# Performance work log

Hardware: AMD Instinct MI355X
Metric: run time of the kernel (lower is better)

The kernel has to match this reference:

```python
import jax, jax.numpy as jnp
import numpy as np

N = 4096      # nodes
DIM = 256     # in/out channels
H = 8         # heads
C = DIM       # per-head channels (PyG TransformerConv: out_channels per head)
EPS = 1e-5    # LayerNorm eps
P_EDGE = 0.01 # adjacency density -> avg in-degree ~41


def setup_inputs() -> dict:
    key = jax.random.key(0)
    ks = jax.random.split(key, 12)
    x = jax.random.normal(ks[0], (1, N, DIM), jnp.float32)
    # sparse random graph encoded densely (dense_to_sparse extracts nonzeros)
    adj_mat = (jax.random.uniform(ks[1], (1, N, N)) < P_EDGE).astype(jnp.float32)
    s = 1.0 / np.sqrt(DIM)
    Wq = jax.random.normal(ks[2], (DIM, H * C), jnp.float32) * s
    Wk = jax.random.normal(ks[3], (DIM, H * C), jnp.float32) * s
    Wv = jax.random.normal(ks[4], (DIM, H * C), jnp.float32) * s
    bq = jax.random.normal(ks[5], (H * C,), jnp.float32) * 0.01
    bk = jax.random.normal(ks[6], (H * C,), jnp.float32) * 0.01
    bv = jax.random.normal(ks[7], (H * C,), jnp.float32) * 0.01
    Wskip = jax.random.normal(ks[8], (DIM, DIM), jnp.float32) * s
    bskip = jax.random.normal(ks[9], (DIM,), jnp.float32) * 0.01
    gamma = jnp.ones((DIM,), jnp.float32)
    beta = jnp.zeros((DIM,), jnp.float32)
    return dict(x=x, adj_mat=adj_mat, Wq=Wq, bq=bq, Wk=Wk, bk=bk, Wv=Wv, bv=bv,
                Wskip=Wskip, bskip=bskip, gamma=gamma, beta=beta)


def reference(x, adj_mat, Wq, bq, Wk, bk, Wv, bv, Wskip, bskip, gamma, beta):
    xs = x[0]            # [N, DIM]
    adj = adj_mat[0]     # [N, N]; adj[j, i] != 0 => edge j -> i (source_to_target)
    q = (xs @ Wq + bq).reshape(N, H, C)
    k = (xs @ Wk + bk).reshape(N, H, C)
    v = (xs @ Wv + bv).reshape(N, H, C)
    # scaled dot-product attention restricted to graph edges
    scores = jnp.einsum('ihc,jhc->hij', q, k) / jnp.sqrt(jnp.float32(C))  # [H,N,N]
    mask = (adj.T != 0.0)[None]  # [1, i_target, j_source]
    neg = jnp.finfo(scores.dtype).min
    attn = jax.nn.softmax(jnp.where(mask, scores, neg), axis=-1)
    # nodes with no in-edges aggregate zero messages (scatter semantics)
    has_nbr = mask.any(axis=-1, keepdims=True)  # [1, N, 1]
    attn = jnp.where(has_nbr, attn, 0.0)
    agg = jnp.einsum('hij,jhc->ihc', attn, v)  # [N, H, C]
    out = agg.mean(axis=1)                      # concat=False -> head mean, [N, DIM]
    out = out + xs @ Wskip + bskip              # root_weight skip connection
    mu = out.mean(axis=-1, keepdims=True)
    var = ((out - mu) ** 2).mean(axis=-1, keepdims=True)
    out = (out - mu) * jax.lax.rsqrt(var + EPS) * gamma + beta  # LayerNorm
    out = out + xs                               # residual
    return out[None]  # [1, N, DIM]
```

## Files before the change

kernel.cpp:

```cpp
#include <hip/hip_runtime.h>
#include <hip/hip_bf16.h>

#define NN   4096
#define DIMM 256
#define HH   8
#define HC   2048
#define CAP  128

#define QSCALE 15.875f
#define SSCALE (0.0625f / (QSCALE * QSCALE))

typedef short    bf16x8 __attribute__((ext_vector_type(8)));
typedef float    f32x4  __attribute__((ext_vector_type(4)));
typedef float    f32x2  __attribute__((ext_vector_type(2)));

__device__ __forceinline__ float bfbits(unsigned int u) {
  union { unsigned int u; float f; } un; un.u = u; return un.f;
}
__device__ __forceinline__ unsigned short f2bf(float f) {
  union { float f; unsigned int u; } un; un.f = f;
  unsigned int r = un.u + 0x7fffu + ((un.u >> 16) & 1u);
  return (unsigned short)(r >> 16);
}
__device__ __forceinline__ int sdot4(unsigned int a, unsigned int b, int c) {
#if __has_builtin(__builtin_amdgcn_sdot4)
  return __builtin_amdgcn_sdot4((int)a, (int)b, c, false);
#else
  c += (int)(signed char)(a)       * (int)(signed char)(b);
  c += (int)(signed char)(a >> 8)  * (int)(signed char)(b >> 8);
  c += (int)(signed char)(a >> 16) * (int)(signed char)(b >> 16);
  c += (int)(signed char)(a >> 24) * (int)(signed char)(b >> 24);
  return c;
#endif
}
__device__ __forceinline__ void gload16(const void* g, void* l) {
  __builtin_amdgcn_global_load_lds(
      (const __attribute__((address_space(1))) unsigned int*)g,
      (__attribute__((address_space(3))) unsigned int*)l, 16, 0, 0);
}

__global__ __launch_bounds__(256) void build_edges_kernel(
    const float4* __restrict__ adj4, int* __restrict__ deg, int* __restrict__ nbr) {
  const int stride = gridDim.x * blockDim.x;
  for (int e4 = blockIdx.x * blockDim.x + threadIdx.x; e4 < NN * NN / 4; e4 += stride) {
    const float4 a = adj4[e4];
    if (a.x != 0.f || a.y != 0.f || a.z != 0.f || a.w != 0.f) {
      const int e = e4 << 2;
      const int j = e >> 12;
      const int ib = e & (NN - 1);
      if (a.x != 0.f) { int s = atomicAdd(&deg[ib + 0], 1); if (s < CAP) nbr[(ib + 0) * CAP + s] = j; }
      if (a.y != 0.f) { int s = atomicAdd(&deg[ib + 1], 1); if (s < CAP) nbr[(ib + 1) * CAP + s] = j; }
      if (a.z != 0.f) { int s = atomicAdd(&deg[ib + 2], 1); if (s < CAP) nbr[(ib + 2) * CAP + s] = j; }
      if (a.w != 0.f) { int s = atomicAdd(&deg[ib + 3], 1); if (s < CAP) nbr[(ib + 3) * CAP + s] = j; }
    }
  }
}

__global__ __launch_bounds__(128) void sort_nbr_kernel(
    const int* __restrict__ deg, int* __restrict__ nbr) {
  const int i = blockIdx.x, t = threadIdx.x;
  __shared__ int sl[CAP];
  int d = deg[i];
  if (d > CAP) d = CAP;
  if (d <= 1) return;
  sl[t] = (t < d) ? nbr[i * CAP + t] : 0x7fffffff;
  __syncthreads();
  for (int ksz = 2; ksz <= CAP; ksz <<= 1) {
    for (int jsz = ksz >> 1; jsz > 0; jsz >>= 1) {
      const int ixj = t ^ jsz;
      if (ixj > t) {
        const int a = sl[t], b = sl[ixj];
        const bool up = ((t & ksz) == 0);
        if ((up && a > b) || (!up && a < b)) { sl[t] = b; sl[ixj] = a; }
      }
      __syncthreads();
    }
  }
  if (t < d) nbr[i * CAP + t] = sl[t];
}

__global__ __launch_bounds__(256) void cast_x_kernel(
    const float* __restrict__ x, unsigned short* __restrict__ xb) {
  const int gid = blockIdx.x * 256 + threadIdx.x;
  const int m = gid >> 5, c = gid & 31;
  const float4 a = *(const float4*)&x[(size_t)m * 256 + c * 8];
  const float4 b = *(const float4*)&x[(size_t)m * 256 + c * 8 + 4];
  union { unsigned short u[8]; uint4 v; } o;
  o.u[0] = f2bf(a.x); o.u[1] = f2bf(a.y); o.u[2] = f2bf(a.z); o.u[3] = f2bf(a.w);
  o.u[4] = f2bf(b.x); o.u[5] = f2bf(b.y); o.u[6] = f2bf(b.z); o.u[7] = f2bf(b.w);
  const int cs = (c & 24) | ((c & 7) ^ (m & 7));
  *(uint4*)&xb[(size_t)m * 256 + cs * 8] = o.v;
}

__global__ __launch_bounds__(256) void tcast_w_kernel(
    const float* __restrict__ W0, const float* __restrict__ W1,
    const float* __restrict__ W2, unsigned short* __restrict__ T0,
    unsigned short* __restrict__ T1, unsigned short* __restrict__ T2, int Nw) {
  const float* W = blockIdx.z == 0 ? W0 : blockIdx.z == 1 ? W1 : W2;
  unsigned short* T = blockIdx.z == 0 ? T0 : blockIdx.z == 1 ? T1 : T2;
  __shared__ float Tf[64][68];
  const int t = threadIdx.x;
  const int n0 = blockIdx.x * 64, k0 = blockIdx.y * 64;
  const int kk0 = t >> 4, nc = t & 15;
#pragma unroll
  for (int r = 0; r < 4; ++r) {
    const int kk = kk0 + r * 16;
    const float4 a = *(const float4*)&W[(size_t)(k0 + kk) * Nw + n0 + nc * 4];
    Tf[kk][nc * 4 + 0] = a.x; Tf[kk][nc * 4 + 1] = a.y;
    Tf[kk][nc * 4 + 2] = a.z; Tf[kk][nc * 4 + 3] = a.w;
  }
  __syncthreads();
  const int n = t >> 2, cp = t & 3;
#pragma unroll
  for (int qq = 0; qq < 2; ++qq) {
    const int cc = cp * 2 + qq;
    union { unsigned short u[8]; uint4 v; } o;
#pragma unroll
    for (int e = 0; e < 8; ++e) o.u[e] = f2bf(Tf[cc * 8 + e][n]);
    const int ng = n0 + n;
    const int co = cc ^ (ng & 7);
    *(uint4*)&T[(size_t)ng * 256 + blockIdx.y * 64 + co * 8] = o.v;
  }
}

template <int MODE>
__global__ __launch_bounds__(256) void mfma_gemm_kernel(
    const unsigned short* __restrict__ Abf,
    const unsigned short* __restrict__ B0, const unsigned short* __restrict__ B1,
    const unsigned short* __restrict__ B2,
    const float* __restrict__ bias0, const float* __restrict__ bias1,
    const float* __restrict__ bias2,
    void* __restrict__ C0v, void* __restrict__ C1v, void* __restrict__ C2v,
    int Nc) {
  const unsigned short* Bm = blockIdx.z == 0 ? B0 : blockIdx.z == 1 ? B1 : B2;
  const float* bias = blockIdx.z == 0 ? bias0 : blockIdx.z == 1 ? bias1 : bias2;
  void* Cv = blockIdx.z == 0 ? C0v : blockIdx.z == 1 ? C1v : C2v;

  __shared__ unsigned short lds[2 * 128 * 64];
  unsigned short* As = lds;
  unsigned short* Bs = lds + 128 * 64;

  const int t = threadIdx.x, l = t & 63, w = t >> 6;
  const int m0 = blockIdx.y * 128, n0 = blockIdx.x * 128;
  const int wm = w >> 1, wn = w & 1;

  const f32x4 zero = {0.f, 0.f, 0.f, 0.f};
  f32x4 acc[4][4];
#pragma unroll
  for (int fm = 0; fm < 4; ++fm)
#pragma unroll
    for (int fn = 0; fn < 4; ++fn) acc[fm][fn] = zero;

  for (int kb = 0; kb < 4; ++kb) {
#pragma unroll
    for (int r = 0; r < 4; ++r) {
      const int rr = r * 8 + (l >> 3), ch = l & 7;
      gload16(Abf + (size_t)(m0 + w * 32 + rr) * 256 + kb * 64 + ch * 8,
              As + w * 2048 + r * 512);
      gload16(Bm + (size_t)(n0 + w * 32 + rr) * 256 + kb * 64 + ch * 8,
              Bs + w * 2048 + r * 512);
    }
    __syncthreads();

#pragma unroll
    for (int s = 0; s < 2; ++s) {
      const int chab = (4 * s + (l >> 4)) ^ (l & 7);
      bf16x8 af[4], bfr[4];
#pragma unroll
      for (int fm = 0; fm < 4; ++fm) {
        const int row = wm * 64 + fm * 16 + (l & 15);
        af[fm] = *(const bf16x8*)&As[row * 64 + chab * 8];
      }
#pragma unroll
      for (int fn = 0; fn < 4; ++fn) {
        const int row = wn * 64 + fn * 16 + (l & 15);
        bfr[fn] = *(const bf16x8*)&Bs[row * 64 + chab * 8];
      }
#pragma unroll
      for (int fm = 0; fm < 4; ++fm)
#pragma unroll
        for (int fn = 0; fn < 4; ++fn)
          acc[fm][fn] = __builtin_amdgcn_mfma_f32_16x16x32_bf16(
              af[fm], bfr[fn], acc[fm][fn], 0, 0, 0);
    }
    __syncthreads();
  }

  float bv[4];
#pragma unroll
  for (int fn = 0; fn < 4; ++fn) bv[fn] = bias[n0 + wn * 64 + fn * 16 + (l & 15)];

  if (MODE == 1) {
    const bool is_i8 = blockIdx.z < 2;
    unsigned char* lds8 = (unsigned char*)lds;
    unsigned char* Cc8 = (unsigned char*)Cv;
#pragma unroll
    for (int fm = 0; fm < 4; ++fm) {
      const int col = wn * 64 + (l & 15);
#pragma unroll
      for (int fn = 0; fn < 4; ++fn) {
#pragma unroll
        for (int r = 0; r < 4; ++r) {
          const int row = wm * 64 + fm * 16 + (l >> 4) * 4 + r;
          const float val = acc[fm][fn][r] + bv[fn];
          unsigned char ob;
          if (is_i8) {
            int vi = (int)rintf(val * QSCALE);
            vi = vi < -127 ? -127 : (vi > 127 ? 127 : vi);
            ob = (unsigned char)(signed char)vi;
          } else {
            const unsigned int pk = __builtin_amdgcn_cvt_pk_fp8_f32(val, val, 0, false);
            ob = (unsigned char)(pk & 0xff);
          }
          lds8[row * 128 + col + fn * 16] = ob;
        }
      }
    }
    __syncthreads();
#pragma unroll
    for (int r2 = 0; r2 < 4; ++r2) {
      const int idx = r2 * 256 + t;
      const int row = idx >> 3, colb = (idx & 7) * 16;
      *(uint4*)&Cc8[(size_t)(m0 + row) * Nc + n0 + colb] =
          *(const uint4*)&lds8[row * 128 + colb];
    }
  } else {
    float* Cc = (float*)Cv;
#pragma unroll
    for (int fm = 0; fm < 4; ++fm)
#pragma unroll
      for (int fn = 0; fn < 4; ++fn)
#pragma unroll
        for (int r = 0; r < 4; ++r) {
          const int row = wm * 64 + fm * 16 + (l >> 4) * 4 + r;
          const int col = wn * 64 + fn * 16 + (l & 15);
          Cc[(size_t)(m0 + row) * Nc + n0 + col] = acc[fm][fn][r] + bv[fn];
        }
  }
}

__global__ __launch_bounds__(256) void attn_ln_kernel(
    const unsigned char* __restrict__ q8, const unsigned char* __restrict__ k8,
    const unsigned char* __restrict__ v8, const float* __restrict__ skip,
    const float* __restrict__ x, const int* __restrict__ deg,
    const int* __restrict__ nbr, const float* __restrict__ gamma,
    const float* __restrict__ beta, float* __restrict__ out) {
  const int i = blockIdx.x;
  const int t = threadIdx.x;
  const int lane = t & 63, wave = t >> 6;
  const int h = lane >> 3, sub = lane & 7;

  __shared__ int slist[CAP];
  __shared__ float sc[CAP * HH];
  __shared__ float wacc[4][2][DIMM];
  __shared__ float mred[HH], lred[HH];
  __shared__ float w1[4], w2[4];

  int d = deg[i];
  if (d > CAP) d = CAP;

  if (t < CAP) slist[t] = (t < d) ? nbr[i * CAP + t] : 0;

  uint4 Q0, Q1;
  {
    const uint4* qp = (const uint4*)&q8[(size_t)i * HC + (h << 8) + (sub << 5)];
    Q0 = qp[0]; Q1 = qp[1];
  }
  __syncthreads();

  {
    const size_t hoff = (size_t)(h << 8) + (sub << 5);
    int n = wave;
    uint4 a0, a1, b0, b1;
    if (n < d) {
      const uint4* kp = (const uint4*)&k8[(size_t)slist[n] * HC + hoff];
      a0 = kp[0]; a1 = kp[1];
    }
    if (n + 4 < d) {
      const uint4* kp = (const uint4*)&k8[(size_t)slist[n + 4] * HC + hoff];
      b0 = kp[0]; b1 = kp[1];
    }
    while (n < d) {
      uint4 c0, c1;
      if (n + 8 < d) {
        const uint4* kp = (const uint4*)&k8[(size_t)slist[n + 8] * HC + hoff];
        c0 = kp[0]; c1 = kp[1];
      }
      int iacc = 0;
      iacc = sdot4(a0.x, Q0.x, iacc); iacc = sdot4(a0.y, Q0.y, iacc);
      iacc = sdot4(a0.z, Q0.z, iacc); iacc = sdot4(a0.w, Q0.w, iacc);
      iacc = sdot4(a1.x, Q1.x, iacc); iacc = sdot4(a1.y, Q1.y, iacc);
      iacc = sdot4(a1.z, Q1.z, iacc); iacc = sdot4(a1.w, Q1.w, iacc);
      float s = (float)iacc;
      s += __shfl_xor(s, 1);
      s += __shfl_xor(s, 2);
      s += __shfl_xor(s, 4);
      if (sub == 0) sc[n * HH + h] = s * SSCALE;
      a0 = b0; a1 = b1; b0 = c0; b1 = c1;
      n += 4;
    }
  }
  __syncthreads();

  if (t < 64) {
    const int h2i = t >> 3, s2 = t & 7;
    float m = -1e30f;
    for (int n2 = s2; n2 < d; n2 += 8) m = fmaxf(m, sc[n2 * HH + h2i]);
    m = fmaxf(m, __shfl_xor(m, 1));
    m = fmaxf(m, __shfl_xor(m, 2));
    m = fmaxf(m, __shfl_xor(m, 4));
    float lsum = 0.f;
    for (int n2 = s2; n2 < d; n2 += 8) lsum += expf(sc[n2 * HH + h2i] - m);
    lsum += __shfl_xor(lsum, 1);
    lsum += __shfl_xor(lsum, 2);
    lsum += __shfl_xor(lsum, 4);
    if (s2 == 0) { mred[h2i] = m; lred[h2i] = (lsum > 0.f) ? 1.f / lsum : 0.f; }
  }
  __syncthreads();

  for (int e = t; e < d * HH; e += 256) {
    const int hh = e & (HH - 1);
    sc[e] = expf(sc[e] - mred[hh]) * lred[hh];
  }
  __syncthreads();

  float a[8] = {0.f, 0.f, 0.f, 0.f, 0.f, 0.f, 0.f, 0.f};
  const int g = lane >> 5, c8 = lane & 31;
  {
    const size_t voff = (size_t)(g * 4) * 256 + (size_t)c8 * 8;
    int n = wave;
    uint2 A0, A1, A2, A3, B0v, B1v, B2v, B3v;
    if (n < d) {
      const unsigned char* vr = &v8[(size_t)slist[n] * HC + voff];
      A0 = *(const uint2*)(vr + 0 * 256); A1 = *(const uint2*)(vr + 1 * 256);
      A2 = *(const uint2*)(vr + 2 * 256); A3 = *(const uint2*)(vr + 3 * 256);
    }
    if (n + 4 < d) {
      const unsigned char* vr = &v8[(size_t)slist[n + 4] * HC + voff];
      B0v = *(const uint2*)(vr + 0 * 256); B1v = *(const uint2*)(vr + 1 * 256);
      B2v = *(const uint2*)(vr + 2 * 256); B3v = *(const uint2*)(vr + 3 * 256);
    }
    while (n < d) {
      uint2 C0, C1, C2, C3;
      if (n + 8 < d) {
        const unsigned char* vr = &v8[(size_t)slist[n + 8] * HC + voff];
        C0 = *(const uint2*)(vr + 0 * 256); C1 = *(const uint2*)(vr + 1 * 256);
        C2 = *(const uint2*)(vr + 2 * 256); C3 = *(const uint2*)(vr + 3 * 256);
      }
      const float p0 = sc[n * HH + g * 4 + 0];
      const float p1 = sc[n * HH + g * 4 + 1];
      const float p2 = sc[n * HH + g * 4 + 2];
      const float p3 = sc[n * HH + g * 4 + 3];
#define AGG_HEAD(w, p)                                                \
      {                                                               \
        const f32x2 u01 = __builtin_amdgcn_cvt_pk_f32_fp8((w).x, false); \
        const f32x2 u23 = __builtin_amdgcn_cvt_pk_f32_fp8((w).x, true);  \
        const f32x2 u45 = __builtin_amdgcn_cvt_pk_f32_fp8((w).y, false); \
        const f32x2 u67 = __builtin_amdgcn_cvt_pk_f32_fp8((w).y, true);  \
        a[0] = fmaf(p, u01[0], a[0]); a[1] = fmaf(p, u01[1], a[1]);   \
        a[2] = fmaf(p, u23[0], a[2]); a[3] = fmaf(p, u23[1], a[3]);   \
        a[4] = fmaf(p, u45[0], a[4]); a[5] = fmaf(p, u45[1], a[5]);   \
        a[6] = fmaf(p, u67[0], a[6]); a[7] = fmaf(p, u67[1], a[7]);   \
      }
      AGG_HEAD(A0, p0) AGG_HEAD(A1, p1) AGG_HEAD(A2, p2) AGG_HEAD(A3, p3)
#undef AGG_HEAD
      A0 = B0v; A1 = B1v; A2 = B2v; A3 = B3v;
      B0v = C0; B1v = C1; B2v = C2; B3v = C3;
      n += 4;
    }
  }
#pragma unroll
  for (int e = 0; e < 8; ++e) wacc[wave][g][c8 * 8 + e] = a[e];
  __syncthreads();

  float accsum = 0.f;
#pragma unroll
  for (int w2 = 0; w2 < 4; ++w2) accsum += wacc[w2][0][t] + wacc[w2][1][t];
  const float oval = accsum * 0.125f + skip[(size_t)i * DIMM + t];

  float s1 = oval, s2 = oval * oval;
#pragma unroll
  for (int off = 32; off > 0; off >>= 1) {
    s1 += __shfl_xor(s1, off, 64);
    s2 += __shfl_xor(s2, off, 64);
  }
  if (lane == 0) { w1[wave] = s1; w2[wave] = s2; }
  __syncthreads();
  const float S1 = w1[0] + w1[1] + w1[2] + w1[3];
  const float S2 = w2[0] + w2[1] + w2[2] + w2[3];
  const float mu = S1 * (1.0f / 256.0f);
  const float var = S2 * (1.0f / 256.0f) - mu * mu;
  const float rst = rsqrtf(var + 1e-5f);

  out[(size_t)i * DIMM + t] =
      (oval - mu) * rst * gamma[t] + beta[t] + x[(size_t)i * DIMM + t];
}

extern "C" void kernel_launch(void* const* d_in, const int* in_sizes, int n_in,
                              void* d_out, int out_size, void* d_ws, size_t ws_size,
                              hipStream_t stream) {
  const float* x     = (const float*)d_in[0];
  const float* adj   = (const float*)d_in[1];
  const float* Wq    = (const float*)d_in[2];
  const float* bq    = (const float*)d_in[3];
  const float* Wk    = (const float*)d_in[4];
  const float* bk    = (const float*)d_in[5];
  const float* Wv    = (const float*)d_in[6];
  const float* bv    = (const float*)d_in[7];
  const float* Wskip = (const float*)d_in[8];
  const float* bskip = (const float*)d_in[9];
  const float* gamma = (const float*)d_in[10];
  const float* beta  = (const float*)d_in[11];
  float* out = (float*)d_out;

  char* ws = (char*)d_ws;
  unsigned short* xb  = (unsigned short*)ws;
  unsigned short* WqT = xb  + (size_t)NN * DIMM;
  unsigned short* WkT = WqT + (size_t)HC * DIMM;
  unsigned short* WvT = WkT + (size_t)HC * DIMM;
  unsigned short* WsT = WvT + (size_t)HC * DIMM;
  float* skip = (float*)(WsT + (size_t)DIMM * DIMM);
  unsigned char* q8 = (unsigned char*)(skip + (size_t)NN * DIMM);
  unsigned char* k8 = q8 + (size_t)NN * HC;
  unsigned char* v8 = k8 + (size_t)NN * HC;
  int* deg = (int*)(v8 + (size_t)NN * HC);
  int* nbr = deg + NN;

  hipMemsetAsync(deg, 0, NN * sizeof(int), stream);
  build_edges_kernel<<<2048, 256, 0, stream>>>((const float4*)adj, deg, nbr);
  sort_nbr_kernel<<<NN, 128, 0, stream>>>(deg, nbr);

  cast_x_kernel<<<NN * 32 / 256, 256, 0, stream>>>(x, xb);
  tcast_w_kernel<<<dim3(HC / 64, 4, 3), 256, 0, stream>>>(Wq, Wk, Wv, WqT, WkT, WvT, HC);
  tcast_w_kernel<<<dim3(DIMM / 64, 4, 1), 256, 0, stream>>>(Wskip, Wskip, Wskip,
                                                            WsT, WsT, WsT, DIMM);

  mfma_gemm_kernel<1><<<dim3(HC / 128, NN / 128, 3), 256, 0, stream>>>(
      xb, WqT, WkT, WvT, bq, bk, bv, q8, k8, v8, HC);
  mfma_gemm_kernel<0><<<dim3(DIMM / 128, NN / 128, 1), 256, 0, stream>>>(
      xb, WsT, WsT, WsT, bskip, bskip, bskip, skip, skip, skip, DIMM);

  attn_ln_kernel<<<NN, 256, 0, stream>>>(q8, k8, v8, skip, x, deg, nbr,
                                         gamma, beta, out);
}
```

Measured before the change: 141.4 us.

## Quantize V to 4-bit and fold skip GEMM into the QKV GEMM launch

Stores V as packed unsigned 4-bit values (scale 1.75, offset 8) instead of fp8. This halves the gather bytes per neighbor in the attention kernel, and the softmax normalization plus a constant correction fold the offset back out. The skip projection GEMM moves into the same launch as a fourth z-slice, with most of its blocks exiting early, which removes one kernel launch. The cost is a large loss of precision in V, which could exceed the accuracy tolerance, and many idle blocks in the fused grid.

```diff
diff --git a/kernel.cpp b/kernel.cpp
--- a/kernel.cpp
+++ b/kernel.cpp
@@ -9,14 +9,13 @@
 
 #define QSCALE 15.875f
 #define SSCALE (0.0625f / (QSCALE * QSCALE))
+#define V4SCALE 1.75f
+#define V4INV  (4.0f / 7.0f)
+#define V4CORR (32.0f / 7.0f)
 
 typedef short    bf16x8 __attribute__((ext_vector_type(8)));
 typedef float    f32x4  __attribute__((ext_vector_type(4)));
-typedef float    f32x2  __attribute__((ext_vector_type(2)));
-
-__device__ __forceinline__ float bfbits(unsigned int u) {
-  union { unsigned int u; float f; } un; un.u = u; return un.f;
-}
+
 __device__ __forceinline__ unsigned short f2bf(float f) {
   union { float f; unsigned int u; } un; un.f = f;
   unsigned int r = un.u + 0x7fffu + ((un.u >> 16) & 1u);
@@ -37,6 +36,12 @@
   __builtin_amdgcn_global_load_lds(
       (const __attribute__((address_space(1))) unsigned int*)g,
       (__attribute__((address_space(3))) unsigned int*)l, 16, 0, 0);
+}
+__device__ __forceinline__ unsigned int pack8n(unsigned int a, unsigned int b) {
+  const unsigned int ya = a | (a >> 4);
+  const unsigned int yb = b | (b >> 4);
+  return (ya & 0xFFu) | ((ya >> 8) & 0xFF00u) |
+         (((yb & 0xFFu) | ((yb >> 8) & 0xFF00u)) << 16);
 }
 
 __global__ __launch_bounds__(256) void build_edges_kernel(
@@ -123,18 +128,20 @@
   }
 }
 
-template <int MODE>
 __global__ __launch_bounds__(256) void mfma_gemm_kernel(
     const unsigned short* __restrict__ Abf,
     const unsigned short* __restrict__ B0, const unsigned short* __restrict__ B1,
-    const unsigned short* __restrict__ B2,
+    const unsigned short* __restrict__ B2, const unsigned short* __restrict__ B3,
     const float* __restrict__ bias0, const float* __restrict__ bias1,
-    const float* __restrict__ bias2,
-    void* __restrict__ C0v, void* __restrict__ C1v, void* __restrict__ C2v,
-    int Nc) {
-  const unsigned short* Bm = blockIdx.z == 0 ? B0 : blockIdx.z == 1 ? B1 : B2;
-  const float* bias = blockIdx.z == 0 ? bias0 : blockIdx.z == 1 ? bias1 : bias2;
-  void* Cv = blockIdx.z == 0 ? C0v : blockIdx.z == 1 ? C1v : C2v;
+    const float* __restrict__ bias2, const float* __restrict__ bias3,
+    void* __restrict__ C0v, void* __restrict__ C1v,
+    void* __restrict__ C2v, void* __restrict__ C3v) {
+  const int z = blockIdx.z;
+  if (z == 3 && blockIdx.x >= 2) return;
+  const unsigned short* Bm = z == 0 ? B0 : z == 1 ? B1 : z == 2 ? B2 : B3;
+  const float* bias = z == 0 ? bias0 : z == 1 ? bias1 : z == 2 ? bias2 : bias3;
+  void* Cv = z == 0 ? C0v : z == 1 ? C1v : z == 2 ? C2v : C3v;
+  const int Nc = (z == 3) ? 256 : 2048;
 
   __shared__ unsigned short lds[2 * 128 * 64];
   unsigned short* As = lds;
@@ -190,8 +197,7 @@
 #pragma unroll
   for (int fn = 0; fn < 4; ++fn) bv[fn] = bias[n0 + wn * 64 + fn * 16 + (l & 15)];
 
-  if (MODE == 1) {
-    const bool is_i8 = blockIdx.z < 2;
+  if (z < 2) {
     unsigned char* lds8 = (unsigned char*)lds;
     unsigned char* Cc8 = (unsigned char*)Cv;
 #pragma unroll
@@ -203,16 +209,9 @@
         for (int r = 0; r < 4; ++r) {
           const int row = wm * 64 + fm * 16 + (l >> 4) * 4 + r;
           const float val = acc[fm][fn][r] + bv[fn];
-          unsigned char ob;
-          if (is_i8) {
-            int vi = (int)rintf(val * QSCALE);
-            vi = vi < -127 ? -127 : (vi > 127 ? 127 : vi);
-            ob = (unsigned char)(signed char)vi;
-          } else {
-            const unsigned int pk = __builtin_amdgcn_cvt_pk_fp8_f32(val, val, 0, false);
-            ob = (unsigned char)(pk & 0xff);
-          }
-          lds8[row * 128 + col + fn * 16] = ob;
+          int vi = (int)rintf(val * QSCALE);
+          vi = vi < -127 ? -127 : (vi > 127 ? 127 : vi);
+          lds8[row * 128 + col + fn * 16] = (unsigned char)(signed char)vi;
         }
       }
     }
@@ -224,6 +223,36 @@
       *(uint4*)&Cc8[(size_t)(m0 + row) * Nc + n0 + colb] =
           *(const uint4*)&lds8[row * 128 + colb];
     }
+  } else if (z == 2) {
+    unsigned char* lds8 = (unsigned char*)lds;
+    unsigned char* Cc8 = (unsigned char*)Cv;
+#pragma unroll
+    for (int fm = 0; fm < 4; ++fm) {
+      const int col = wn * 64 + (l & 15);
+#pragma unroll
+      for (int fn = 0; fn < 4; ++fn) {
+#pragma unroll
+        for (int r = 0; r < 4; ++r) {
+          const int row = wm * 64 + fm * 16 + (l >> 4) * 4 + r;
+          const float val = acc[fm][fn][r] + bv[fn];
+          int vi = (int)rintf(val * V4SCALE) + 8;
+          vi = vi < 0 ? 0 : (vi > 15 ? 15 : vi);
+          lds8[row * 128 + col + fn * 16] = (unsigned char)vi;
+        }
+      }
+    }
+    __syncthreads();
+#pragma unroll
+    for (int u2 = 0; u2 < 2; ++u2) {
+      const int unit = u2 * 256 + t;
+      const int row = unit >> 2, ch = unit & 3;
+      const uint4 x0 = *(const uint4*)&lds8[row * 128 + ch * 32];
+      const uint4 x1 = *(const uint4*)&lds8[row * 128 + ch * 32 + 16];
+      uint4 o;
+      o.x = pack8n(x0.x, x0.y); o.y = pack8n(x0.z, x0.w);
+      o.z = pack8n(x1.x, x1.y); o.w = pack8n(x1.z, x1.w);
+      *(uint4*)&Cc8[(size_t)(m0 + row) * 1024 + (n0 >> 1) + ch * 16] = o;
+    }
   } else {
     float* Cc = (float*)Cv;
 #pragma unroll
@@ -241,7 +270,7 @@
 
 __global__ __launch_bounds__(256) void attn_ln_kernel(
     const unsigned char* __restrict__ q8, const unsigned char* __restrict__ k8,
-    const unsigned char* __restrict__ v8, const float* __restrict__ skip,
+    const unsigned char* __restrict__ v4, const float* __restrict__ skip,
     const float* __restrict__ x, const int* __restrict__ deg,
     const int* __restrict__ nbr, const float* __restrict__ gamma,
     const float* __restrict__ beta, float* __restrict__ out) {
@@ -314,7 +343,7 @@
     lsum += __shfl_xor(lsum, 1);
     lsum += __shfl_xor(lsum, 2);
     lsum += __shfl_xor(lsum, 4);
-    if (s2 == 0) { mred[h2i] = m; lred[h2i] = (lsum > 0.f) ? 1.f / lsum : 0.f; }
+    if (s2 == 0) { mred[h2i] = m; lred[h2i] = (lsum > 0.f) ? V4INV / lsum : 0.f; }
   }
   __syncthreads();
 
@@ -327,45 +356,47 @@
   float a[8] = {0.f, 0.f, 0.f, 0.f, 0.f, 0.f, 0.f, 0.f};
   const int g = lane >> 5, c8 = lane & 31;
   {
-    const size_t voff = (size_t)(g * 4) * 256 + (size_t)c8 * 8;
+    const size_t voff = (size_t)(g * 4) * 128 + (size_t)c8 * 4;
     int n = wave;
-    uint2 A0, A1, A2, A3, B0v, B1v, B2v, B3v;
+    unsigned int A0, A1, A2, A3, B0w, B1w, B2w, B3w;
     if (n < d) {
-      const unsigned char* vr = &v8[(size_t)slist[n] * HC + voff];
-      A0 = *(const uint2*)(vr + 0 * 256); A1 = *(const uint2*)(vr + 1 * 256);
-      A2 = *(const uint2*)(vr + 2 * 256); A3 = *(const uint2*)(vr + 3 * 256);
+      const unsigned char* vr = &v4[(size_t)slist[n] * 1024 + voff];
+      A0 = *(const unsigned int*)(vr + 0 * 128); A1 = *(const unsigned int*)(vr + 1 * 128);
+      A2 = *(const unsigned int*)(vr + 2 * 128); A3 = *(const unsigned int*)(vr + 3 * 128);
     }
     if (n + 4 < d) {
-      const unsigned char* vr = &v8[(size_t)slist[n + 4] * HC + voff];
-      B0v = *(const uint2*)(vr + 0 * 256); B1v = *(const uint2*)(vr + 1 * 256);
-      B2v = *(const uint2*)(vr + 2 * 256); B3v = *(const uint2*)(vr + 3 * 256);
+      const unsigned char* vr = &v4[(size_t)slist[n + 4] * 1024 + voff];
+      B0w = *(const unsigned int*)(vr + 0 * 128); B1w = *(const unsigned int*)(vr + 1 * 128);
+      B2w = *(const unsigned int*)(vr + 2 * 128); B3w = *(const unsigned int*)(vr + 3 * 128);
     }
     while (n < d) {
-      uint2 C0, C1, C2, C3;
+      unsigned int C0, C1, C2, C3;
       if (n + 8 < d) {
-        const unsigned char* vr = &v8[(size_t)slist[n + 8] * HC + voff];
-        C0 = *(const uint2*)(vr + 0 * 256); C1 = *(const uint2*)(vr + 1 * 256);
-        C2 = *(const uint2*)(vr + 2 * 256); C3 = *(const uint2*)(vr + 3 * 256);
+        const unsigned char* vr = &v4[(size_t)slist[n + 8] * 1024 + voff];
+        C0 = *(const unsigned int*)(vr + 0 * 128); C1 = *(const unsigned int*)(vr + 1 * 128);
+        C2 = *(const unsigned int*)(vr + 2 * 128); C3 = *(const unsigned int*)(vr + 3 * 128);
       }
       const float p0 = sc[n * HH + g * 4 + 0];
       const float p1 = sc[n * HH + g * 4 + 1];
       const float p2 = sc[n * HH + g * 4 + 2];
       const float p3 = sc[n * HH + g * 4 + 3];
-#define AGG_HEAD(w, p)                                                \
-      {                                                               \
-        const f32x2 u01 = __builtin_amdgcn_cvt_pk_f32_fp8((w).x, false); \
-        const f32x2 u23 = __builtin_amdgcn_cvt_pk_f32_fp8((w).x, true);  \
-        const f32x2 u45 = __builtin_amdgcn_cvt_pk_f32_fp8((w).y, false); \
-        const f32x2 u67 = __builtin_amdgcn_cvt_pk_f32_fp8((w).y, true);  \
-        a[0] = fmaf(p, u01[0], a[0]); a[1] = fmaf(p, u01[1], a[1]);   \
-        a[2] = fmaf(p, u23[0], a[2]); a[3] = fmaf(p, u23[1], a[3]);   \
-        a[4] = fmaf(p, u45[0], a[4]); a[5] = fmaf(p, u45[1], a[5]);   \
-        a[6] = fmaf(p, u67[0], a[6]); a[7] = fmaf(p, u67[1], a[7]);   \
-      }
-      AGG_HEAD(A0, p0) AGG_HEAD(A1, p1) AGG_HEAD(A2, p2) AGG_HEAD(A3, p3)
-#undef AGG_HEAD
-      A0 = B0v; A1 = B1v; A2 = B2v; A3 = B3v;
-      B0v = C0; B1v = C1; B2v = C2; B3v = C3;
+#define AGG4(w, p)                                                     \
+      {                                                                \
+        const unsigned int lo = (w) & 0x0F0F0F0Fu;                     \
+        const unsigned int hi = ((w) >> 4) & 0x0F0F0F0Fu;              \
+        a[0] = fmaf(p, (float)(lo & 0xFFu), a[0]);                     \
+        a[1] = fmaf(p, (float)(hi & 0xFFu), a[1]);                     \
+        a[2] = fmaf(p, (float)((lo >> 8) & 0xFFu), a[2]);              \
+        a[3] = fmaf(p, (float)((hi >> 8) & 0xFFu), a[3]);              \
+        a[4] = fmaf(p, (float)((lo >> 16) & 0xFFu), a[4]);             \
+        a[5] = fmaf(p, (float)((hi >> 16) & 0xFFu), a[5]);             \
+        a[6] = fmaf(p, (float)(lo >> 24), a[6]);                       \
+        a[7] = fmaf(p, (float)(hi >> 24), a[7]);                       \
+      }
+      AGG4(A0, p0) AGG4(A1, p1) AGG4(A2, p2) AGG4(A3, p3)
+#undef AGG4
+      A0 = B0w; A1 = B1w; A2 = B2w; A3 = B3w;
+      B0w = C0; B1w = C1; B2w = C2; B3w = C3;
       n += 4;
     }
   }
@@ -376,7 +407,8 @@
   float accsum = 0.f;
 #pragma unroll
   for (int w2 = 0; w2 < 4; ++w2) accsum += wacc[w2][0][t] + wacc[w2][1][t];
-  const float oval = accsum * 0.125f + skip[(size_t)i * DIMM + t];
+  const float corr = (d > 0) ? V4CORR : 0.f;
+  const float oval = accsum * 0.125f - corr + skip[(size_t)i * DIMM + t];
 
   float s1 = oval, s2 = oval * oval;
 #pragma unroll
@@ -422,8 +454,8 @@
   float* skip = (float*)(WsT + (size_t)DIMM * DIMM);
   unsigned char* q8 = (unsigned char*)(skip + (size_t)NN * DIMM);
   unsigned char* k8 = q8 + (size_t)NN * HC;
-  unsigned char* v8 = k8 + (size_t)NN * HC;
-  int* deg = (int*)(v8 + (size_t)NN * HC);
+  unsigned char* v4 = k8 + (size_t)NN * HC;
+  int* deg = (int*)(v4 + (size_t)NN * 1024);
   int* nbr = deg + NN;
 
   hipMemsetAsync(deg, 0, NN * sizeof(int), stream);
@@ -435,11 +467,9 @@
   tcast_w_kernel<<<dim3(DIMM / 64, 4, 1), 256, 0, stream>>>(Wskip, Wskip, Wskip,
                                                             WsT, WsT, WsT, DIMM);
 
-  mfma_gemm_kernel<1><<<dim3(HC / 128, NN / 128, 3), 256, 0, stream>>>(
-      xb, WqT, WkT, WvT, bq, bk, bv, q8, k8, v8, HC);
-  mfma_gemm_kernel<0><<<dim3(DIMM / 128, NN / 128, 1), 256, 0, stream>>>(
-      xb, WsT, WsT, WsT, bskip, bskip, bskip, skip, skip, skip, DIMM);
-
-  attn_ln_kernel<<<NN, 256, 0, stream>>>(q8, k8, v8, skip, x, deg, nbr,
+  mfma_gemm_kernel<<<dim3(HC / 128, NN / 128, 4), 256, 0, stream>>>(
+      xb, WqT, WkT, WvT, WsT, bq, bk, bv, bskip, q8, k8, v4, skip);
+
+  attn_ln_kernel<<<NN, 256, 0, stream>>>(q8, k8, v4, skip, x, deg, nbr,
                                          gamma, beta, out);
 }
```

Result: no change. 139.7 us (-1.2%).
